# Optimization experiments

Hardware: AMD Instinct MI355X
Metric: run time of the kernel (lower is better)

The kernel has to match this reference:

```python
import jax, jax.numpy as jnp
import numpy as np

K = 3          # kernel_size
STRIDE = 1
ITERS = 3      # num_iterations


def squash(t, axis=-1):
    sn = jnp.sum(t * t, axis=axis, keepdims=True)
    return (sn / (1.0 + sn)) * t / jnp.sqrt(sn)


def setup_inputs() -> dict:
    key = jax.random.key(0)
    k1, k2 = jax.random.split(key)
    B, Nin, H, Cin = 8, 32, 14, 8
    C, Cout = 32, 16
    R = Nin * K * K  # 288 route nodes
    x = jax.random.normal(k1, (B, Nin, H, H, Cin), dtype=jnp.float32)
    route_weights = jax.random.normal(k2, (C, R, Cin, Cout), dtype=jnp.float32)
    return {"x": x, "route_weights": route_weights}


def reference(x, route_weights):
    B, Nin, H, _, Cin = x.shape
    C, R, _, Cout = route_weights.shape
    w = (H - K) // STRIDE + 1

    # Extract all w*w spatial windows at once (instead of the python loop).
    rows = STRIDE * jnp.arange(w)[:, None] + jnp.arange(K)  # [w, K]
    win = x[:, :, rows]            # [B, Nin, w, K, W, Cin]
    win = win[:, :, :, :, rows]    # [B, Nin, w, K, w, K, Cin]
    # route-node order matches .view: (Nin, k, k) flattened
    win = win.transpose(0, 2, 4, 1, 3, 5, 6).reshape(B, w, w, R, Cin)

    priors = jnp.einsum('bpqri,crio->cbpqro', win, route_weights)

    # Dynamic routing (fixed small iteration count -> python loop is fine).
    logits = jnp.zeros_like(priors)
    out = None
    for i in range(ITERS):
        probs = jax.nn.softmax(logits, axis=4)  # softmax over route nodes (dim=2 in torch 5D layout)
        out = squash(jnp.sum(probs * priors, axis=4, keepdims=True))  # [C,B,w,w,1,Cout]
        if i != ITERS - 1:
            logits = logits + jnp.sum(priors * out, axis=-1, keepdims=True)

    out = out[:, :, :, :, 0, :]          # [C, B, w, w, Cout]
    return out.transpose(1, 0, 2, 3, 4)  # [B, C, w, w, Cout]
```

## Files before the change

kernel.cpp:

```cpp
#include <hip/hip_runtime.h>
#include <math.h>

namespace {
constexpr int B_    = 8;
constexpr int NIN   = 32;
constexpr int H_    = 14;
constexpr int CIN   = 8;
constexpr int C_    = 32;
constexpr int COUT  = 16;
constexpr int R_    = 288;
constexpr int W_    = 12;
constexpr int NITER = 3;
constexpr int CH    = 32;
constexpr int NCH   = 9;
constexpr size_t XSUB = (size_t)NIN * H_ * H_ * CIN;
}

typedef unsigned int u32;
typedef const __attribute__((address_space(1))) u32* as1_u32p;
typedef __attribute__((address_space(3))) u32* as3_u32p;

__device__ __forceinline__ void async_copy16(const void* g, void* l) {
    __builtin_amdgcn_global_load_lds((as1_u32p)g, (as3_u32p)l, 16, 0, 0);
}
__device__ __forceinline__ float dot4(const float4 a, const float4 b) {
    return fmaf(a.x, b.x, fmaf(a.y, b.y, fmaf(a.z, b.z, a.w * b.w)));
}

__device__ __forceinline__ float dpp_add_xor1(float v) {
    int t = __builtin_amdgcn_update_dpp(0, __float_as_int(v), 0xB1, 0xF, 0xF, true);
    return v + __int_as_float(t);
}
__device__ __forceinline__ float dpp_add_xor2(float v) {
    int t = __builtin_amdgcn_update_dpp(0, __float_as_int(v), 0x4E, 0xF, 0xF, true);
    return v + __int_as_float(t);
}

__global__ __launch_bounds__(256)
void caps_route9(const float* __restrict__ x,
                 const float* __restrict__ rw,
                 float* __restrict__ out)
{
    const int tid = threadIdx.x;
    const int p  = blockIdx.x / W_;
    const int q  = blockIdx.x % W_;
    const int b0 = blockIdx.y * 4;
    const int c  = blockIdx.z;

    __shared__ float4 wbuf[2][1024];
    __shared__ float4 xbuf[2][256];
    __shared__ float  sRed[4][2][16];
    __shared__ float  redE[4][2];
    __shared__ float  vS[4][16];

    const int og   = tid & 3;
    const int rl   = tid >> 2;
    const int cr   = rl & 31;
    const int sh   = rl >> 5;
    const int lane = tid & 63;
    const int wv   = tid >> 6;

    const float* x0 = x + (size_t)b0 * XSUB;
    const float4* rwcF4 = (const float4*)(rw + (size_t)c * R_ * CIN * COUT);

    const int xsub  = wv;
    const int xhalf = (tid >> 5) & 1;
    const int xcr   = tid & 31;

    float4 acc[NCH][2];

    auto stage = [&](int k, int buf) {
        const float4* gchunk = rwcF4 + (size_t)k * (CH * 32);
        #pragma unroll
        for (int t = 0; t < 4; ++t) {
            const int s   = t * 256 + tid;
            const int ii  = s >> 7;
            const int wcr = (s >> 2) & 31;
            async_copy16(gchunk + (wcr * 32 + ii * 4 + (s & 3)),
                         (char*)&wbuf[buf][0] + (t * 256 + (tid & 192)) * 16);
        }
        const int r  = k * CH + xcr;
        const int n  = r / 9, rem = r - n * 9;
        const int kh = rem / 3, kw = rem - kh * 3;
        const float* xp = x0 + (size_t)xsub * XSUB
                        + ((n * H_ + (p + kh)) * H_ + (q + kw)) * CIN + xhalf * 4;
        async_copy16(xp, (char*)&xbuf[buf][0] + (tid & 192) * 16);
    };

    stage(0, 0);
    #pragma unroll
    for (int k = 0; k < NCH; ++k) {
        __syncthreads();
        if (k + 1 < NCH) stage(k + 1, (k + 1) & 1);
        const int buf = k & 1;
        const float4* wb  = &wbuf[buf][0];
        const float4* xbp = &xbuf[buf][0];
        const float4 xA0 = xbp[sh * 128 + cr];
        const float4 xA1 = xbp[sh * 128 + 32 + cr];
        const float4 xB0 = xbp[sh * 128 + 64 + cr];
        const float4 xB1 = xbp[sh * 128 + 96 + cr];
        const float fA[8] = {xA0.x, xA0.y, xA0.z, xA0.w, xA1.x, xA1.y, xA1.z, xA1.w};
        const float fB[8] = {xB0.x, xB0.y, xB0.z, xB0.w, xB1.x, xB1.y, xB1.z, xB1.w};
        float4 a0 = make_float4(0.f, 0.f, 0.f, 0.f);
        float4 a1 = make_float4(0.f, 0.f, 0.f, 0.f);
        #pragma unroll
        for (int i = 0; i < 8; ++i) {
            const float4 wv4 = wb[i * 128 + cr * 4 + og];
            a0.x = fmaf(fA[i], wv4.x, a0.x);  a1.x = fmaf(fB[i], wv4.x, a1.x);
            a0.y = fmaf(fA[i], wv4.y, a0.y);  a1.y = fmaf(fB[i], wv4.y, a1.y);
            a0.z = fmaf(fA[i], wv4.z, a0.z);  a1.z = fmaf(fB[i], wv4.z, a1.z);
            a0.w = fmaf(fA[i], wv4.w, a0.w);  a1.w = fmaf(fB[i], wv4.w, a1.w);
        }
        acc[k][0] = a0;  acc[k][1] = a1;
    }

    const int sA = sh * 2;
    float lgA[NCH], lgB[NCH];
    #pragma unroll
    for (int j = 0; j < NCH; ++j) { lgA[j] = 0.f; lgB[j] = 0.f; }

    for (int it = 0; it < NITER; ++it) {
        float4 s0 = make_float4(0.f, 0.f, 0.f, 0.f);
        float4 s1 = make_float4(0.f, 0.f, 0.f, 0.f);
        float se0 = 0.f, se1 = 0.f;

        if (it == 0) {
            #pragma unroll
            for (int j = 0; j < NCH; ++j) {
                s0.x += acc[j][0].x;  s1.x += acc[j][1].x;
                s0.y += acc[j][0].y;  s1.y += acc[j][1].y;
                s0.z += acc[j][0].z;  s1.z += acc[j][1].z;
                s0.w += acc[j][0].w;  s1.w += acc[j][1].w;
            }
        } else {
            const float4 v0 = *(const float4*)&vS[sA][og * 4];
            const float4 v1 = *(const float4*)&vS[sA + 1][og * 4];
            #pragma unroll
            for (int j = 0; j < NCH; ++j) {
                float d0 = dot4(acc[j][0], v0);
                float d1 = dot4(acc[j][1], v1);
                d0 = dpp_add_xor1(d0);  d1 = dpp_add_xor1(d1);
                d0 = dpp_add_xor2(d0);  d1 = dpp_add_xor2(d1);
                lgA[j] += d0;                 lgB[j] += d1;
                const float e0 = __expf(lgA[j]);
                const float e1 = __expf(lgB[j]);
                se0 += e0;                    se1 += e1;
                s0.x = fmaf(e0, acc[j][0].x, s0.x);  s1.x = fmaf(e1, acc[j][1].x, s1.x);
                s0.y = fmaf(e0, acc[j][0].y, s0.y);  s1.y = fmaf(e1, acc[j][1].y, s1.y);
                s0.z = fmaf(e0, acc[j][0].z, s0.z);  s1.z = fmaf(e1, acc[j][1].z, s1.z);
                s0.w = fmaf(e0, acc[j][0].w, s0.w);  s1.w = fmaf(e1, acc[j][1].w, s1.w);
            }
            #pragma unroll
            for (int off = 4; off <= 32; off <<= 1) {
                se0 += __shfl_xor(se0, off, 64);
                se1 += __shfl_xor(se1, off, 64);
            }
            if (lane == 0) { redE[wv][0] = se0; redE[wv][1] = se1; }
        }

        #pragma unroll
        for (int off = 4; off <= 32; off <<= 1) {
            s0.x += __shfl_xor(s0.x, off, 64);  s1.x += __shfl_xor(s1.x, off, 64);
            s0.y += __shfl_xor(s0.y, off, 64);  s1.y += __shfl_xor(s1.y, off, 64);
            s0.z += __shfl_xor(s0.z, off, 64);  s1.z += __shfl_xor(s1.z, off, 64);
            s0.w += __shfl_xor(s0.w, off, 64);  s1.w += __shfl_xor(s1.w, off, 64);
        }
        if (lane < 4) {
            *(float4*)&sRed[wv][0][lane * 4] = s0;
            *(float4*)&sRed[wv][1][lane * 4] = s1;
        }
        __syncthreads();

        if (tid < 64) {
            const int sub = tid >> 4;
            const int o   = tid & 15;
            const int g   = sub >> 1;
            const int l   = sub & 1;
            const float inv = (it == 0)
                ? (1.0f / (float)R_)
                : 1.0f / (redE[g * 2][l] + redE[g * 2 + 1][l]);
            float s = (sRed[g * 2][l][o] + sRed[g * 2 + 1][l][o]) * inv;
            float sn = s * s;
            sn = dpp_add_xor1(sn);
            sn = dpp_add_xor2(sn);
            sn += __shfl_xor(sn, 4, 64);
            sn += __shfl_xor(sn, 8, 64);
            const float v = s * (sqrtf(sn) / (1.0f + sn));
            if (it == NITER - 1) {
                out[((((size_t)(b0 + sub) * C_ + c) * W_ + p) * W_ + q) * COUT + o] = v;
            } else {
                vS[sub][o] = v;
            }
        }
        if (it == NITER - 1) break;
        __syncthreads();
    }
}

extern "C" void kernel_launch(void* const* d_in, const int* in_sizes, int n_in,
                              void* d_out, int out_size, void* d_ws, size_t ws_size,
                              hipStream_t stream) {
    const float* x  = (const float*)d_in[0];
    const float* rw = (const float*)d_in[1];
    float* out = (float*)d_out;
    dim3 grid(W_ * W_, B_ / 4, C_);
    caps_route9<<<grid, 256, 0, stream>>>(x, rw, out);
}
```

Before: 205.1 us.

## Process all eight batches per block and load inputs directly to registers

Each block now covers all 8 batch elements with 512 threads instead of 4 batches with 256, so each route-weight chunk staged into LDS is reused across twice as many batches and half as many blocks reload it. Input windows are now read straight from global memory into registers and prefetched one chunk ahead, replacing the async LDS staging for x. This halves the grid and removes redundant weight traffic, but it gives fewer blocks to spread across CUs and raises per-block register pressure.

New measurement: 242.8 us. +18.4%, slower.

```diff
diff --git a/kernel.cpp b/kernel.cpp
--- a/kernel.cpp
+++ b/kernel.cpp
@@ -2,7 +2,6 @@
 #include <math.h>
 
 namespace {
-constexpr int B_    = 8;
 constexpr int NIN   = 32;
 constexpr int H_    = 14;
 constexpr int CIN   = 8;
@@ -26,7 +25,6 @@
 __device__ __forceinline__ float dot4(const float4 a, const float4 b) {
     return fmaf(a.x, b.x, fmaf(a.y, b.y, fmaf(a.z, b.z, a.w * b.w)));
 }
-
 __device__ __forceinline__ float dpp_add_xor1(float v) {
     int t = __builtin_amdgcn_update_dpp(0, __float_as_int(v), 0xB1, 0xF, 0xF, true);
     return v + __int_as_float(t);
@@ -36,71 +34,64 @@
     return v + __int_as_float(t);
 }
 
-__global__ __launch_bounds__(256)
-void caps_route9(const float* __restrict__ x,
+__global__ __launch_bounds__(512)
+void caps_routeA(const float* __restrict__ x,
                  const float* __restrict__ rw,
                  float* __restrict__ out)
 {
     const int tid = threadIdx.x;
     const int p  = blockIdx.x / W_;
     const int q  = blockIdx.x % W_;
-    const int b0 = blockIdx.y * 4;
-    const int c  = blockIdx.z;
+    const int c  = blockIdx.y;
 
     __shared__ float4 wbuf[2][1024];
-    __shared__ float4 xbuf[2][256];
-    __shared__ float  sRed[4][2][16];
-    __shared__ float  redE[4][2];
-    __shared__ float  vS[4][16];
+    __shared__ float  sRed[8][2][16];
+    __shared__ float  redE[8][2];
+    __shared__ float  vS[8][16];
 
     const int og   = tid & 3;
-    const int rl   = tid >> 2;
-    const int cr   = rl & 31;
-    const int sh   = rl >> 5;
+    const int cr   = (tid >> 2) & 31;
     const int lane = tid & 63;
     const int wv   = tid >> 6;
+    const int sA   = (tid >> 7) * 2;
 
-    const float* x0 = x + (size_t)b0 * XSUB;
+    const float* xA = x + (size_t)sA * XSUB;
     const float4* rwcF4 = (const float4*)(rw + (size_t)c * R_ * CIN * COUT);
 
-    const int xsub  = wv;
-    const int xhalf = (tid >> 5) & 1;
-    const int xcr   = tid & 31;
-
-    float4 acc[NCH][2];
+    float4 xv0, xv1, xv2, xv3;
+    auto xld = [&](int k) {
+        const int r  = k * CH + cr;
+        const int n  = r / 9, rem = r - n * 9;
+        const int kh = rem / 3, kw = rem - kh * 3;
+        const float* xp = xA + ((n * H_ + (p + kh)) * H_ + (q + kw)) * CIN;
+        xv0 = *(const float4*)xp;          xv1 = *(const float4*)(xp + 4);
+        xv2 = *(const float4*)(xp + XSUB); xv3 = *(const float4*)(xp + XSUB + 4);
+    };
 
     auto stage = [&](int k, int buf) {
         const float4* gchunk = rwcF4 + (size_t)k * (CH * 32);
         #pragma unroll
-        for (int t = 0; t < 4; ++t) {
-            const int s   = t * 256 + tid;
+        for (int t = 0; t < 2; ++t) {
+            const int s   = t * 512 + tid;
             const int ii  = s >> 7;
             const int wcr = (s >> 2) & 31;
             async_copy16(gchunk + (wcr * 32 + ii * 4 + (s & 3)),
-                         (char*)&wbuf[buf][0] + (t * 256 + (tid & 192)) * 16);
+                         (char*)&wbuf[buf][0] + (t * 512 + (tid & 448)) * 16);
         }
-        const int r  = k * CH + xcr;
-        const int n  = r / 9, rem = r - n * 9;
-        const int kh = rem / 3, kw = rem - kh * 3;
-        const float* xp = x0 + (size_t)xsub * XSUB
-                        + ((n * H_ + (p + kh)) * H_ + (q + kw)) * CIN + xhalf * 4;
-        async_copy16(xp, (char*)&xbuf[buf][0] + (tid & 192) * 16);
     };
 
+    float4 acc[NCH][2];
+
+    xld(0);
     stage(0, 0);
     #pragma unroll
     for (int k = 0; k < NCH; ++k) {
         __syncthreads();
         if (k + 1 < NCH) stage(k + 1, (k + 1) & 1);
-        const int buf = k & 1;
-        const float4* wb  = &wbuf[buf][0];
-        const float4* xbp = &xbuf[buf][0];
-        const float4 xA0 = xbp[sh * 128 + cr];
-        const float4 xA1 = xbp[sh * 128 + 32 + cr];
-        const float4 xB0 = xbp[sh * 128 + 64 + cr];
-        const float4 xB1 = xbp[sh * 128 + 96 + cr];
-        const float fA[8] = {xA0.x, xA0.y, xA0.z, xA0.w, xA1.x, xA1.y, xA1.z, xA1.w};
-        const float fB[8] = {xB0.x, xB0.y, xB0.z, xB0.w, xB1.x, xB1.y, xB1.z, xB1.w};
+        const float4* wb = &wbuf[k & 1][0];
+        const float fA[8] = {xv0.x, xv0.y, xv0.z, xv0.w, xv1.x, xv1.y, xv1.z, xv1.w};
+        const float fB[8] = {xv2.x, xv2.y, xv2.z, xv2.w, xv3.x, xv3.y, xv3.z, xv3.w};
+        if (k + 1 < NCH) xld(k + 1);
         float4 a0 = make_float4(0.f, 0.f, 0.f, 0.f);
         float4 a1 = make_float4(0.f, 0.f, 0.f, 0.f);
         #pragma unroll
@@ -114,7 +105,6 @@
         acc[k][0] = a0;  acc[k][1] = a1;
     }
 
-    const int sA = sh * 2;
     float lgA[NCH], lgB[NCH];
     #pragma unroll
     for (int j = 0; j < NCH; ++j) { lgA[j] = 0.f; lgB[j] = 0.f; }
@@ -171,7 +161,7 @@
         }
         __syncthreads();
 
-        if (tid < 64) {
+        if (tid < 128) {
             const int sub = tid >> 4;
             const int o   = tid & 15;
             const int g   = sub >> 1;
@@ -187,7 +177,7 @@
             sn += __shfl_xor(sn, 8, 64);
             const float v = s * (sqrtf(sn) / (1.0f + sn));
             if (it == NITER - 1) {
-                out[((((size_t)(b0 + sub) * C_ + c) * W_ + p) * W_ + q) * COUT + o] = v;
+                out[((((size_t)sub * C_ + c) * W_ + p) * W_ + q) * COUT + o] = v;
             } else {
                 vS[sub][o] = v;
             }
@@ -203,6 +193,6 @@
     const float* x  = (const float*)d_in[0];
     const float* rw = (const float*)d_in[1];
     float* out = (float*)d_out;
-    dim3 grid(W_ * W_, B_ / 4, C_);
-    caps_route9<<<grid, 256, 0, stream>>>(x, rw, out);
+    dim3 grid(W_ * W_, C_);
+    caps_routeA<<<grid, 512, 0, stream>>>(x, rw, out);
 }
```
